# Performance work log

Measured on AMD Instinct MI355X. Metric: run time of the kernel, lower is better.

## Reference

```python
import jax, jax.numpy as jnp
import numpy as np

N = 100000       # nodes
E = 3200000      # edges (avg degree 32)
IN_FEATS = 128
HIDDEN = 32
PROP_STEP = 8
USE_RELU = False  # args.relu default


def setup_inputs() -> dict:
    key = jax.random.key(0)
    k1, k2, k3, k4, k5 = jax.random.split(key, 5)
    in_feat = jax.random.normal(k1, (N, IN_FEATS), jnp.float32)
    src = jax.random.randint(k2, (E,), 0, N)
    dst = jax.random.randint(k3, (E,), 0, N)
    # Glorot-ish uniform init like DGL GraphConv weights
    s1 = float(np.sqrt(6.0 / (IN_FEATS + HIDDEN)))
    s2 = float(np.sqrt(6.0 / (HIDDEN + HIDDEN)))
    W1 = jax.random.uniform(k4, (IN_FEATS, HIDDEN), jnp.float32, -s1, s1)
    b1 = jnp.zeros((HIDDEN,), jnp.float32)
    W2 = jax.random.uniform(k5, (HIDDEN, HIDDEN), jnp.float32, -s2, s2)
    b2 = jnp.zeros((HIDDEN,), jnp.float32)
    return {"in_feat": in_feat, "W1": W1, "b1": b1, "W2": W2, "b2": b2,
            "src": src, "dst": dst}


def _graph_conv(x, W, b, src, dst, out_norm, in_norm, weight_first):
    # DGL GraphConv, norm='both':
    #   h = x * out_deg^{-1/2}; (optionally h @ W); SpMM aggregate src->dst;
    #   rst = agg * in_deg^{-1/2}; (optionally @ W); + bias
    h = x * out_norm[:, None]
    if weight_first:
        h = h @ W  # [N, out]
    agg = jax.ops.segment_sum(h[src], dst, num_segments=x.shape[0])
    rst = agg * in_norm[:, None]
    if not weight_first:
        rst = rst @ W
    return rst + b


def reference(in_feat, W1, b1, W2, b2, src, dst):
    n = in_feat.shape[0]
    ones = jnp.ones((src.shape[0],), in_feat.dtype)
    out_deg = jax.ops.segment_sum(ones, src, num_segments=n)
    in_deg = jax.ops.segment_sum(ones, dst, num_segments=n)
    out_norm = jax.lax.rsqrt(jnp.maximum(out_deg, 1.0))
    in_norm = jax.lax.rsqrt(jnp.maximum(in_deg, 1.0))
    # conv1: in_feats(128) > out_feats(32) -> weight applied before aggregation
    h = _graph_conv(in_feat, W1, b1, src, dst, out_norm, in_norm, weight_first=True)
    for _ in range(1, PROP_STEP):
        if USE_RELU:
            h = jax.nn.relu(h)
        h = _graph_conv(h, W2, b2, src, dst, out_norm, in_norm, weight_first=False)
    return h
```

## Files before the change

### kernel.cpp

```cpp
#include <hip/hip_runtime.h>
#include <hip/hip_bf16.h>

#define NNODES 100000
#define NEDGES 3200000
#define INF 128
#define HID 32
#define NB 392
#define BSHIFT 8
#define NPB 256
#define BATCH 8192
#define PART_BLOCKS ((NEDGES + BATCH - 1) / BATCH)

typedef unsigned short u16;

__device__ __forceinline__ float blo(unsigned x) { return __uint_as_float(x << 16); }
__device__ __forceinline__ float bhi(unsigned x) { return __uint_as_float(x & 0xffff0000u); }
__device__ __forceinline__ u16 f2b(float f) {
    __hip_bfloat16 h = __float2bfloat16(f);
    return *reinterpret_cast<u16*>(&h);
}

__global__ void k_cnt(const int* __restrict__ src, const int* __restrict__ dst,
                      int* __restrict__ bcnt_src, int* __restrict__ bcnt_dst) {
    __shared__ int hs[NB], hd[NB];
    int tid = threadIdx.x;
    for (int i = tid; i < NB; i += 1024) { hs[i] = 0; hd[i] = 0; }
    __syncthreads();
    int start = blockIdx.x * BATCH;
    int end = start + BATCH; if (end > NEDGES) end = NEDGES;
    for (int i = start + tid; i < end; i += 1024) {
        atomicAdd(&hs[src[i] >> BSHIFT], 1);
        atomicAdd(&hd[dst[i] >> BSHIFT], 1);
    }
    __syncthreads();
    for (int i = tid; i < NB; i += 1024) {
        if (hs[i]) atomicAdd(&bcnt_src[i], hs[i]);
        if (hd[i]) atomicAdd(&bcnt_dst[i], hd[i]);
    }
}

__global__ void k_bscan(const int* __restrict__ bcnt_src, const int* __restrict__ bcnt_dst,
                        int* __restrict__ bbase_src, int* __restrict__ bbase_dst,
                        int* __restrict__ gcur_src, int* __restrict__ gcur_dst) {
    __shared__ int s[512], t[512];
    int tid = threadIdx.x;
    int vs = (tid < NB) ? bcnt_src[tid] : 0;
    int vd = (tid < NB) ? bcnt_dst[tid] : 0;
    s[tid] = vs; t[tid] = vd;
    __syncthreads();
    for (int off = 1; off < 512; off <<= 1) {
        int a = (tid >= off) ? s[tid - off] : 0;
        int b = (tid >= off) ? t[tid - off] : 0;
        __syncthreads();
        s[tid] += a; t[tid] += b;
        __syncthreads();
    }
    if (tid < NB) {
        bbase_src[tid] = s[tid] - vs;  gcur_src[tid] = s[tid] - vs;
        bbase_dst[tid] = t[tid] - vd;  gcur_dst[tid] = t[tid] - vd;
    }
}

__global__ void k_bucket2(const int* __restrict__ src, const int* __restrict__ dst,
                          int* __restrict__ gcur_src, int* __restrict__ gcur_dst,
                          int2* __restrict__ pairbuf, int* __restrict__ srctmp) {
    __shared__ int2 stage2[BATCH];
    __shared__ int cnt[NB], excl[NB], gbase[NB];
    __shared__ int sc[512];
    int* stage1 = (int*)stage2;
    int tid = threadIdx.x;
    int start = blockIdx.x * BATCH;
    int end = start + BATCH; if (end > NEDGES) end = NEDGES;
    int cntE = end - start;

    int dd[8], sv[8], rk[8];

    for (int i = tid; i < NB; i += 1024) cnt[i] = 0;
    __syncthreads();
#pragma unroll
    for (int k = 0; k < 8; ++k) {
        int i = start + tid + k * 1024;
        dd[k] = -1;
        if (i < end) {
            dd[k] = dst[i]; sv[k] = src[i];
            rk[k] = atomicAdd(&cnt[dd[k] >> BSHIFT], 1);
        }
    }
    __syncthreads();
    if (tid < 512) sc[tid] = (tid < NB) ? cnt[tid] : 0;
    __syncthreads();
    for (int off = 1; off < 512; off <<= 1) {
        int v = (tid < 512 && tid >= off) ? sc[tid - off] : 0;
        __syncthreads();
        if (tid < 512) sc[tid] += v;
        __syncthreads();
    }
    if (tid < NB) {
        excl[tid] = sc[tid] - cnt[tid];
        int c = cnt[tid];
        gbase[tid] = c ? atomicAdd(&gcur_dst[tid], c) : 0;
    }
    __syncthreads();
#pragma unroll
    for (int k = 0; k < 8; ++k)
        if (dd[k] >= 0) {
            int2 e; e.x = dd[k]; e.y = sv[k];
            stage2[excl[dd[k] >> BSHIFT] + rk[k]] = e;
        }
    __syncthreads();
    for (int j = tid; j < cntE; j += 1024) {
        int2 e = stage2[j];
        int b = e.x >> BSHIFT;
        pairbuf[gbase[b] + (j - excl[b])] = e;
    }
    __syncthreads();

    for (int i = tid; i < NB; i += 1024) cnt[i] = 0;
    __syncthreads();
#pragma unroll
    for (int k = 0; k < 8; ++k)
        if (dd[k] >= 0)
            rk[k] = atomicAdd(&cnt[sv[k] >> BSHIFT], 1);
    __syncthreads();
    if (tid < 512) sc[tid] = (tid < NB) ? cnt[tid] : 0;
    __syncthreads();
    for (int off = 1; off < 512; off <<= 1) {
        int v = (tid < 512 && tid >= off) ? sc[tid - off] : 0;
        __syncthreads();
        if (tid < 512) sc[tid] += v;
        __syncthreads();
    }
    if (tid < NB) {
        excl[tid] = sc[tid] - cnt[tid];
        int c = cnt[tid];
        gbase[tid] = c ? atomicAdd(&gcur_src[tid], c) : 0;
    }
    __syncthreads();
#pragma unroll
    for (int k = 0; k < 8; ++k)
        if (dd[k] >= 0)
            stage1[excl[sv[k] >> BSHIFT] + rk[k]] = sv[k];
    __syncthreads();
    for (int j = tid; j < cntE; j += 1024) {
        int v = stage1[j];
        int b = v >> BSHIFT;
        srctmp[gbase[b] + (j - excl[b])] = v;
    }
}

__global__ void k_nodes(const int* __restrict__ srctmp, const int2* __restrict__ pairbuf,
                        const int* __restrict__ bbase_src, const int* __restrict__ bcnt_src,
                        const int* __restrict__ bbase_dst, const int* __restrict__ bcnt_dst,
                        float* __restrict__ out_norm, float* __restrict__ in_norm,
                        int* __restrict__ indeg, int* __restrict__ rowstart) {
    __shared__ int cnt[NPB];
    __shared__ int ss[NPB];
    int tid = threadIdx.x;
    int b = blockIdx.x;
    int srcphase = (b < NB);
    int bb = srcphase ? b : b - NB;
    int node0 = bb * NPB;
    cnt[tid] = 0;
    __syncthreads();
    if (srcphase) {
        int s0 = bbase_src[bb], n = bcnt_src[bb];
        for (int i = tid; i < n; i += 256)
            atomicAdd(&cnt[srctmp[s0 + i] - node0], 1);
        __syncthreads();
        int nn = node0 + tid;
        if (nn < NNODES) {
            int c = cnt[tid];
            out_norm[nn] = rsqrtf((float)(c > 1 ? c : 1));
        }
    } else {
        int d0 = bbase_dst[bb], n = bcnt_dst[bb];
        for (int i = tid; i < n; i += 256)
            atomicAdd(&cnt[pairbuf[d0 + i].x - node0], 1);
        __syncthreads();
        int c = cnt[tid];
        ss[tid] = c;
        __syncthreads();
        for (int off = 1; off < 256; off <<= 1) {
            int t = (tid >= off) ? ss[tid - off] : 0;
            __syncthreads();
            ss[tid] += t;
            __syncthreads();
        }
        int excl = ss[tid] - c;
        int nn = node0 + tid;
        if (nn < NNODES) {
            indeg[nn] = c;
            in_norm[nn] = rsqrtf((float)(c > 1 ? c : 1));
            rowstart[nn] = d0 + excl;
        }
    }
}

__global__ void k_place(const int2* __restrict__ pairbuf, const int* __restrict__ rowstart,
                        int* __restrict__ col) {
    __shared__ int cur[NPB];
    int tid = threadIdx.x;
    int bucket = blockIdx.x;
    int node0 = bucket * NPB;
    if (node0 >= NNODES) return;
    int n = node0 + tid;
    cur[tid] = (n < NNODES) ? rowstart[n] : 0;
    __syncthreads();
    int pstart = rowstart[node0];
    int pend   = (node0 + NPB >= NNODES) ? NEDGES : rowstart[node0 + NPB];
    for (int i = pstart + tid; i < pend; i += 256) {
        int2 e = pairbuf[i];
        int pos = atomicAdd(&cur[e.x - node0], 1);
        col[pos] = e.y;
    }
}

__global__ void k_gemm1(const float* __restrict__ x, const float* __restrict__ W1,
                        const float* __restrict__ out_norm, u16* __restrict__ t) {
    __shared__ float wlds[INF * HID];
    __shared__ float xlds[8][INF];
    int tid = threadIdx.x;
    for (int i = tid; i < INF * HID; i += 256) wlds[i] = W1[i];
    int group = tid >> 5, lane = tid & 31;
    int row = blockIdx.x * 8 + group;
    float4 xv = ((const float4*)(x + (size_t)row * INF))[lane];
    ((float4*)xlds[group])[lane] = xv;
    __syncthreads();
    float acc = 0.f;
#pragma unroll
    for (int k = 0; k < INF; ++k)
        acc += xlds[group][k] * wlds[k * HID + lane];
    t[(size_t)row * HID + lane] = f2b(acc * out_norm[row]);
}

template<int APPLY_W, int FINAL>
__global__ void k_spmm(const u16* __restrict__ gin, const int* __restrict__ rowstart,
                       const int* __restrict__ indeg, const int* __restrict__ col,
                       const float* __restrict__ in_norm, const float* __restrict__ out_norm,
                       const float* __restrict__ W, const float* __restrict__ bias,
                       void* __restrict__ gout) {
    __shared__ float wlds[HID * HID];
    __shared__ float sh[8][HID];
    int tid = threadIdx.x, lane = tid & 31, group = tid >> 5;
    int g = lane >> 2, f = lane & 3;
    if (APPLY_W) {
        for (int i = tid; i < HID * HID; i += 256) wlds[i] = W[i];
        __syncthreads();
    }
    int n = blockIdx.x * 8 + group;
    int start = rowstart[n];
    int deg   = indeg[n];
    const uint4* gin16 = (const uint4*)gin;

    float a[8];
#pragma unroll
    for (int j = 0; j < 8; ++j) a[j] = 0.f;

    int base = 0;
    for (; base + 32 <= deg; base += 32) {
        int c = col[start + base + lane];
#pragma unroll
        for (int t = 0; t < 4; ++t) {
            int s = __shfl(c, t * 8 + g, 32);
            uint4 v = gin16[(size_t)s * 4 + f];
            a[0] += blo(v.x); a[1] += bhi(v.x);
            a[2] += blo(v.y); a[3] += bhi(v.y);
            a[4] += blo(v.z); a[5] += bhi(v.z);
            a[6] += blo(v.w); a[7] += bhi(v.w);
        }
    }
    if (base < deg) {
        int rem = deg - base;
        int c = (base + lane < deg) ? col[start + base + lane] : 0;
#pragma unroll
        for (int t = 0; t < 4; ++t) {
            if (t * 8 < rem) {
                int e = t * 8 + g;
                int s = __shfl(c, e, 32);
                uint4 v = gin16[(size_t)s * 4 + f];
                float m = (e < rem) ? 1.f : 0.f;
                a[0] = fmaf(m, blo(v.x), a[0]); a[1] = fmaf(m, bhi(v.x), a[1]);
                a[2] = fmaf(m, blo(v.y), a[2]); a[3] = fmaf(m, bhi(v.y), a[3]);
                a[4] = fmaf(m, blo(v.z), a[4]); a[5] = fmaf(m, bhi(v.z), a[5]);
                a[6] = fmaf(m, blo(v.w), a[6]); a[7] = fmaf(m, bhi(v.w), a[7]);
            }
        }
    }
#pragma unroll
    for (int j = 0; j < 8; ++j) {
        a[j] += __shfl_xor(a[j], 4, 32);
        a[j] += __shfl_xor(a[j], 8, 32);
        a[j] += __shfl_xor(a[j], 16, 32);
    }
    float inm = in_norm[n];
    if (g == 0) {
        float4 lo = make_float4(a[0] * inm, a[1] * inm, a[2] * inm, a[3] * inm);
        float4 hi = make_float4(a[4] * inm, a[5] * inm, a[6] * inm, a[7] * inm);
        *(float4*)&sh[group][f * 8]     = lo;
        *(float4*)&sh[group][f * 8 + 4] = hi;
    }
    float res;
    if (APPLY_W) {
        float o = bias[lane];
#pragma unroll
        for (int k = 0; k < HID; ++k)
            o += sh[group][k] * wlds[k * HID + lane];
        res = o;
    } else {
        res = sh[group][lane] + bias[lane];
    }
    if (FINAL) ((float*)gout)[(size_t)n * HID + lane] = res;
    else       ((u16*)gout)[(size_t)n * HID + lane] = f2b(res * out_norm[n]);
}

extern "C" void kernel_launch(void* const* d_in, const int* in_sizes, int n_in,
                              void* d_out, int out_size, void* d_ws, size_t ws_size,
                              hipStream_t stream) {
    const float* in_feat = (const float*)d_in[0];
    const float* W1      = (const float*)d_in[1];
    const float* b1      = (const float*)d_in[2];
    const float* W2      = (const float*)d_in[3];
    const float* b2      = (const float*)d_in[4];
    const int*   src     = (const int*)d_in[5];
    const int*   dst     = (const int*)d_in[6];
    float*       out     = (float*)d_out;

    const int N = NNODES, E = NEDGES;
    int* bcnt_src  = (int*)d_ws;
    int* bcnt_dst  = bcnt_src + 512;
    int* bbase_src = bcnt_dst + 512;
    int* bbase_dst = bbase_src + 512;
    int* gcur_src  = bbase_dst + 512;
    int* gcur_dst  = gcur_src + 512;
    int* indeg     = gcur_dst + 512;
    int* rowstart  = indeg + N;
    float* out_norm = (float*)(rowstart + N);
    float* in_norm  = out_norm + N;
    int*   col      = (int*)(in_norm + N);
    void*  bufreg   = (void*)(col + E);
    int2*  pairbuf  = (int2*)bufreg;
    int*   srctmp   = col;
    u16*   bufA16   = (u16*)bufreg;
    u16*   bufB16   = bufA16 + (size_t)N * HID;
    size_t need = ((size_t)3072 + 4 * N + E + (size_t)2 * N * HID) * 4;
    if (ws_size < need) return;

    hipMemsetAsync(bcnt_src, 0, 1024 * sizeof(int), stream);

    k_cnt    <<<PART_BLOCKS, 1024, 0, stream>>>(src, dst, bcnt_src, bcnt_dst);
    k_bscan  <<<1, 512, 0, stream>>>(bcnt_src, bcnt_dst, bbase_src, bbase_dst,
                                     gcur_src, gcur_dst);
    k_bucket2<<<PART_BLOCKS, 1024, 0, stream>>>(src, dst, gcur_src, gcur_dst,
                                                pairbuf, srctmp);
    k_nodes  <<<2 * NB, 256, 0, stream>>>(srctmp, pairbuf, bbase_src, bcnt_src,
                                          bbase_dst, bcnt_dst, out_norm, in_norm,
                                          indeg, rowstart);
    k_place  <<<NB, 256, 0, stream>>>(pairbuf, rowstart, col);

    k_gemm1<<<N / 8, 256, 0, stream>>>(in_feat, W1, out_norm, bufA16);

    k_spmm<0, 0><<<N / 8, 256, 0, stream>>>(bufA16, rowstart, indeg, col, in_norm,
                                            out_norm, W2, b1, bufB16);

    u16* cur = bufB16; u16* nxt = bufA16;
    for (int i = 0; i < 6; ++i) {
        k_spmm<1, 0><<<N / 8, 256, 0, stream>>>(cur, rowstart, indeg, col, in_norm,
                                                out_norm, W2, b2, nxt);
        u16* tmp = cur; cur = nxt; nxt = tmp;
    }
    k_spmm<1, 1><<<N / 8, 256, 0, stream>>>(cur, rowstart, indeg, col, in_norm,
                                            out_norm, W2, b2, out);
}
```

Measured before the change: 480.8 us.

## Register-tile first-layer GEMM with 256-row blocks and transposed LDS staging

Rewrites the dense 128x32 projection kernel so each block handles 256 rows. Each thread computes a 4x8 register tile from transposed x chunks staged in LDS over 16-wide K slices, then writes packed bf16 with vector stores. The goal is to reload W1 into LDS far less often and raise FMA work per LDS read. The cost is fewer blocks (about 391) and more registers per thread.

Result: faster. 465.6 us (median of 2 runs) (-3.2%).

```diff
diff --git a/kernel.cpp b/kernel.cpp
--- a/kernel.cpp
+++ b/kernel.cpp
@@ -10,6 +10,9 @@
 #define NPB 256
 #define BATCH 8192
 #define PART_BLOCKS ((NEDGES + BATCH - 1) / BATCH)
+#define G1_ROWS 256
+#define G1_KC 16
+#define G1_XP 260
 
 typedef unsigned short u16;
 
@@ -215,22 +218,73 @@
     }
 }
 
-__global__ void k_gemm1(const float* __restrict__ x, const float* __restrict__ W1,
-                        const float* __restrict__ out_norm, u16* __restrict__ t) {
+__global__ __launch_bounds__(256) void k_gemm1(const float* __restrict__ x,
+                                               const float* __restrict__ W1,
+                                               const float* __restrict__ out_norm,
+                                               u16* __restrict__ t) {
     __shared__ float wlds[INF * HID];
-    __shared__ float xlds[8][INF];
-    int tid = threadIdx.x;
+    __shared__ float xT[G1_KC][G1_XP];
+    int tid = threadIdx.x;
+    int row0 = blockIdx.x * G1_ROWS;
     for (int i = tid; i < INF * HID; i += 256) wlds[i] = W1[i];
-    int group = tid >> 5, lane = tid & 31;
-    int row = blockIdx.x * 8 + group;
-    float4 xv = ((const float4*)(x + (size_t)row * INF))[lane];
-    ((float4*)xlds[group])[lane] = xv;
-    __syncthreads();
-    float acc = 0.f;
-#pragma unroll
-    for (int k = 0; k < INF; ++k)
-        acc += xlds[group][k] * wlds[k * HID + lane];
-    t[(size_t)row * HID + lane] = f2b(acc * out_norm[row]);
+
+    int rg = tid >> 2;
+    int cg = tid & 3;
+    int sr = tid >> 2;
+    int kq = tid & 3;
+
+    float acc[4][8];
+#pragma unroll
+    for (int r = 0; r < 4; ++r)
+#pragma unroll
+        for (int c = 0; c < 8; ++c) acc[r][c] = 0.f;
+
+    for (int kc = 0; kc < INF; kc += G1_KC) {
+#pragma unroll
+        for (int pass = 0; pass < 4; ++pass) {
+            int r = pass * 64 + sr;
+            int grow = row0 + r;
+            float4 xv = make_float4(0.f, 0.f, 0.f, 0.f);
+            if (grow < NNODES)
+                xv = *(const float4*)(x + (size_t)grow * INF + kc + kq * 4);
+            xT[kq * 4 + 0][r] = xv.x;
+            xT[kq * 4 + 1][r] = xv.y;
+            xT[kq * 4 + 2][r] = xv.z;
+            xT[kq * 4 + 3][r] = xv.w;
+        }
+        __syncthreads();
+#pragma unroll
+        for (int kk = 0; kk < G1_KC; ++kk) {
+            float4 xr = *(const float4*)&xT[kk][rg * 4];
+            float4 wa = *(const float4*)&wlds[(kc + kk) * HID + cg * 8];
+            float4 wb = *(const float4*)&wlds[(kc + kk) * HID + cg * 8 + 4];
+            float xs[4] = {xr.x, xr.y, xr.z, xr.w};
+#pragma unroll
+            for (int r = 0; r < 4; ++r) {
+                acc[r][0] = fmaf(xs[r], wa.x, acc[r][0]);
+                acc[r][1] = fmaf(xs[r], wa.y, acc[r][1]);
+                acc[r][2] = fmaf(xs[r], wa.z, acc[r][2]);
+                acc[r][3] = fmaf(xs[r], wa.w, acc[r][3]);
+                acc[r][4] = fmaf(xs[r], wb.x, acc[r][4]);
+                acc[r][5] = fmaf(xs[r], wb.y, acc[r][5]);
+                acc[r][6] = fmaf(xs[r], wb.z, acc[r][6]);
+                acc[r][7] = fmaf(xs[r], wb.w, acc[r][7]);
+            }
+        }
+        __syncthreads();
+    }
+#pragma unroll
+    for (int r = 0; r < 4; ++r) {
+        int row = row0 + rg * 4 + r;
+        if (row < NNODES) {
+            float on = out_norm[row];
+            unsigned p0 = f2b(acc[r][0] * on) | ((unsigned)f2b(acc[r][1] * on) << 16);
+            unsigned p1 = f2b(acc[r][2] * on) | ((unsigned)f2b(acc[r][3] * on) << 16);
+            unsigned p2 = f2b(acc[r][4] * on) | ((unsigned)f2b(acc[r][5] * on) << 16);
+            unsigned p3 = f2b(acc[r][6] * on) | ((unsigned)f2b(acc[r][7] * on) << 16);
+            *(uint4*)(t + (size_t)row * HID + cg * 8) = make_uint4(p0, p1, p2, p3);
+        }
+    }
 }
 
 template<int APPLY_W, int FINAL>
@@ -357,7 +411,7 @@
                                           indeg, rowstart);
     k_place  <<<NB, 256, 0, stream>>>(pairbuf, rowstart, col);
 
-    k_gemm1<<<N / 8, 256, 0, stream>>>(in_feat, W1, out_norm, bufA16);
+    k_gemm1<<<(N + G1_ROWS - 1) / G1_ROWS, 256, 0, stream>>>(in_feat, W1, out_norm, bufA16);
 
     k_spmm<0, 0><<<N / 8, 256, 0, stream>>>(bufA16, rowstart, indeg, col, in_norm,
                                             out_norm, W2, b1, bufB16);
```
